# Kernel optimization log

Measured on AMD Instinct MI355X. Metric: run time of the kernel, lower is better.

The kernel has to match this reference:

```python
import jax, jax.numpy as jnp
import numpy as np

B, T, D, H, C = 64, 512, 128, 512, 256  # batch, seq_len, input_dim, rnn_dim, clf hidden


def _lstm_cell(x, h, c, Wih, Whh, b):
    # PyTorch gate order: i, f, g, o; b = bias_ih + bias_hh
    gates = x @ Wih.T + h @ Whh.T + b  # [B, 4H]
    i, f, g, o = jnp.split(gates, 4, axis=-1)
    c = jax.nn.sigmoid(f) * c + jax.nn.sigmoid(i) * jnp.tanh(g)
    h = jax.nn.sigmoid(o) * jnp.tanh(c)
    return h, c


def _run_lstm2(xs, state, p0, p1):
    # xs: [B, T, in]; state: (h0, c0, h1, c1) each [B, H]
    def step(carry, x_t):
        h0, c0, h1, c1 = carry
        h0, c0 = _lstm_cell(x_t, h0, c0, *p0)
        h1, c1 = _lstm_cell(h0, h1, c1, *p1)
        return (h0, c0, h1, c1), h1
    state, ys = jax.lax.scan(step, state, jnp.swapaxes(xs, 0, 1))
    return jnp.swapaxes(ys, 0, 1), state


def setup_inputs() -> dict:
    key = jax.random.key(0)
    ks = jax.random.split(key, 18)
    s = 0.04  # ~1/sqrt(H), matches torch LSTM init scale
    w = lambda k, shape: (jax.random.normal(k, shape, jnp.float32) * s)
    inp = {
        "x": jax.random.uniform(ks[0], (B, T, D), dtype=jnp.float32),
        "y": (jax.random.uniform(ks[1], (B, T, D), dtype=jnp.float32) > 0.9).astype(jnp.float32),
        "enc_Wih0": w(ks[2], (4 * H, D)), "enc_Whh0": w(ks[3], (4 * H, H)), "enc_b0": w(ks[4], (4 * H,)),
        "enc_Wih1": w(ks[5], (4 * H, H)), "enc_Whh1": w(ks[6], (4 * H, H)), "enc_b1": w(ks[7], (4 * H,)),
        "dec_Wih0": w(ks[8], (4 * H, D)), "dec_Whh0": w(ks[9], (4 * H, H)), "dec_b0": w(ks[10], (4 * H,)),
        "dec_Wih1": w(ks[11], (4 * H, H)), "dec_Whh1": w(ks[12], (4 * H, H)), "dec_b1": w(ks[13], (4 * H,)),
        "clf_W1": w(ks[14], (C, H)), "clf_b1": w(ks[15], (C,)),
        "clf_W2": w(ks[16], (D, C)), "clf_b2": w(ks[17], (D,)),
    }
    return inp


def reference(x, y, enc_Wih0, enc_Whh0, enc_b0, enc_Wih1, enc_Whh1, enc_b1,
              dec_Wih0, dec_Whh0, dec_b0, dec_Wih1, dec_Whh1, dec_b1,
              clf_W1, clf_b1, clf_W2, clf_b2):
    Bc = x.shape[0]
    z = jnp.zeros((Bc, H), x.dtype)
    # encoder: only final (h, c) of both layers is used
    _, state = _run_lstm2(x, (z, z, z, z),
                          (enc_Wih0, enc_Whh0, enc_b0), (enc_Wih1, enc_Whh1, enc_b1))
    # decoder under full teacher forcing: steps t=1..T-1 consume y[:, t-1]
    dec_out, _ = _run_lstm2(y[:, :-1], state,
                            (dec_Wih0, dec_Whh0, dec_b0), (dec_Wih1, dec_Whh1, dec_b1))
    hid = jax.nn.relu(dec_out @ clf_W1.T + clf_b1)          # [B, T-1, C]
    logits = hid @ clf_W2.T + clf_b2                        # [B, T-1, D]
    # outputs[:, 0] stays zero, as in the torch loop starting at t=1
    return jnp.concatenate([jnp.zeros_like(logits[:, :1]), logits], axis=1)
```

## Files before the change

### kernel.cpp

```cpp
#include <hip/hip_runtime.h>
#include <hip/hip_bf16.h>
#include <stdint.h>

#define SMEM_BYTES 150528

using short8  = __attribute__((ext_vector_type(8))) short;
using f32x4   = __attribute__((ext_vector_type(4))) float;
using u32x4   = __attribute__((ext_vector_type(4))) unsigned int;

#define OXBF 0u
#define OYBF 8388608u
#define OWE0 16777216u
#define OWD0 (OWE0 + 2621440u)
#define OWE1 (OWD0 + 2621440u)
#define OWD1 (OWE1 + 4194304u)
#define OWC1 (OWD1 + 4194304u)
#define OWC2 (OWC1 + 262144u)
#define OH0  (OWC2 + 65536u)
#define OH1  (OH0 + 524288u)
#define OHP  (OH1 + 524288u)
#define OFLG (OHP + 262144u)
#define OFC1 (OFLG + 4096u)
#define OFH  (OFLG + 8192u)
#define OFL  (OFLG + 9216u)
#define OH1B (OFLG + 16384u)

static __device__ __forceinline__ unsigned short f2bf(float f){
  union { float f; unsigned u; } v; v.f = f;
  unsigned r = v.u + 0x7FFFu + ((v.u >> 16) & 1u);
  return (unsigned short)(r >> 16);
}
static __device__ __forceinline__ float sigm(float x){ return 1.f/(1.f+__expf(-x)); }
static __device__ __forceinline__ float tanh_(float x){ return 1.f - 2.f/(__expf(2.f*x)+1.f); }

static __device__ __forceinline__ u32x4 ld_cg16(const void* p){
  u32x4 v;
  asm volatile("global_load_dwordx4 %0, %1, off sc0 sc1" : "=v"(v) : "v"(p) : "memory");
  return v;
}
static __device__ __forceinline__ unsigned ld_cg4(const void* p){
  unsigned v;
  asm volatile("global_load_dword %0, %1, off sc0 sc1\n\ts_waitcnt vmcnt(0)"
               : "=v"(v) : "v"(p) : "memory");
  return v;
}
static __device__ __forceinline__ void st_cg16(void* p, u32x4 v){
  asm volatile("global_store_dwordx4 %0, %1, off sc0 sc1" :: "v"(p), "v"(v) : "memory");
}
static __device__ __forceinline__ void st_cg4(void* p, unsigned v){
  asm volatile("global_store_dword %0, %1, off sc0 sc1" :: "v"(p), "v"(v) : "memory");
}
static __device__ __forceinline__ void drain_vm(){
  asm volatile("s_waitcnt vmcnt(0)" ::: "memory");
}
static __device__ __forceinline__ bool isS(u32x4 v){
  return (v[0]==0xFFFFFFFFu) | (v[1]==0xFFFFFFFFu) | (v[2]==0xFFFFFFFFu) | (v[3]==0xFFFFFFFFu);
}

__global__ void k_init(float* __restrict__ out, uint8_t* __restrict__ ws){
  int i = blockIdx.x*blockDim.x + threadIdx.x;
  int ns = gridDim.x*blockDim.x;
  uint32_t* r0 = (uint32_t*)(ws + OH0);
  uint32_t* r1 = (uint32_t*)(ws + OH1);
  const int slotw = 65536/4;
  for (int k=i; k<8*slotw; k+=ns){
    unsigned v = (k < 7*slotw) ? 0xFFFFFFFFu : 0u;
    r0[k] = v; r1[k] = v;
  }
  uint32_t* rb = (uint32_t*)(ws + OH1B);
  for (int k=i; k<8*slotw; k+=ns) rb[k] = 0xFFFFFFFFu;
  uint32_t* rp = (uint32_t*)(ws + OHP);
  for (int k=i; k<262144/4; k+=ns) rp[k] = 0xFFFFFFFFu;
  uint32_t* fl = (uint32_t*)(ws + OFLG);
  for (int k=i; k<16384/4; k+=ns) fl[k] = 0u;
  for (int k=i; k<64*128; k+=ns) out[(size_t)(k>>7)*(512*128) + (k&127)] = 0.f;
}

__global__ void k_cvt(const float* __restrict__ x, const float* __restrict__ y,
                      uint8_t* __restrict__ ws){
  unsigned short* xb = (unsigned short*)(ws + OXBF);
  unsigned short* yb = (unsigned short*)(ws + OYBF);
  const int n = 64*512*128;
  int i = blockIdx.x*blockDim.x + threadIdx.x, ns = gridDim.x*blockDim.x;
  for (int k=i; k<n; k+=ns){ xb[k] = f2bf(x[k]); yb[k] = f2bf(y[k]); }
}

__global__ void k_swzgate(const float* __restrict__ Wih, const float* __restrict__ Whh,
                          uint8_t* __restrict__ ws, size_t dstOff, int Kin, int KC, int NKK, int mode){
  unsigned short* dst = (unsigned short*)(ws + dstOff);
  const int total = 2048 * (KC*4);
  int i = blockIdx.x*blockDim.x + threadIdx.x, ns = gridDim.x*blockDim.x;
  for (int idx=i; idx<total; idx+=ns){
    int j = idx & 7;
    int lane = (idx >> 3) & 63;
    int t = idx >> 9;
    int g = t & 3; t >>= 2;
    int kk = t % NKK; t /= NKK;
    int w = t & 3; int ub = t >> 2;
    int off = ((lane>>4)<<3) + j;
    int k = mode ? (kk==0 ? w*32 + off : 128 + w*128 + (kk-1)*32 + off)
                 : (w*KC + kk*32 + off);
    int u = ub*16 + (lane&15);
    int row = g*512 + u;
    float v = (k < Kin) ? Wih[(size_t)row*Kin + k] : Whh[(size_t)row*512 + (k-Kin)];
    dst[idx] = f2bf(v);
  }
}

__global__ void k_swzclf(const float* __restrict__ W, uint8_t* __restrict__ ws,
                         size_t dstOff, int nwgs, int Kw, int Ktot){
  unsigned short* dst = (unsigned short*)(ws + dstOff);
  const int NKK = Kw/32;
  const int total = nwgs*4*NKK*64*8;
  int i = blockIdx.x*blockDim.x + threadIdx.x, ns = gridDim.x*blockDim.x;
  for (int idx=i; idx<total; idx+=ns){
    int j = idx & 7;
    int lane = (idx >> 3) & 63;
    int t = idx >> 9;
    int kk = t % NKK; t /= NKK;
    int w = t & 3; int wg = t >> 2;
    int k = w*Kw + kk*32 + ((lane>>4)<<3) + j;
    int col = wg*16 + (lane&15);
    dst[idx] = f2bf(W[(size_t)col*Ktot + k]);
  }
}

__launch_bounds__(256, 1)
__global__ void k_seq(uint8_t* __restrict__ ws,
                      const float* __restrict__ eb0, const float* __restrict__ eb1,
                      const float* __restrict__ db0, const float* __restrict__ db1,
                      const float* __restrict__ cb1, const float* __restrict__ cb2,
                      float* __restrict__ out){
  __shared__ uint8_t smem[SMEM_BYTES];
  const int wg = blockIdx.x, tid = threadIdx.x;
  const int w = tid>>6, l = tid&63, lr = l&15, lg = l>>4;

  const unsigned short* xb = (const unsigned short*)(ws+OXBF);
  const unsigned short* yb = (const unsigned short*)(ws+OYBF);
  unsigned short* h0r = (unsigned short*)(ws+OH0);
  unsigned short* h1r = (unsigned short*)(ws+OH1);
  unsigned short* h1b = (unsigned short*)(ws+OH1B);
  unsigned short* hpr = (unsigned short*)(ws+OHP);

  short8* BL = (short8*)smem;
  float*  P0 = (float*)(smem + 131072);
  float*  P1 = (float*)(smem + 139776);
  unsigned short* HS = (unsigned short*)(smem + 148480);

  const u32x4 S4 = (u32x4){0xFFFFFFFFu,0xFFFFFFFFu,0xFFFFFFFFu,0xFFFFFFFFu};

  auto loadB = [&](size_t srcOff, int bytes){
    const u32x4* s = (const u32x4*)(ws + srcOff);
    u32x4* d = (u32x4*)smem;
    for (int i = tid; i < bytes/16; i += 256) d[i] = s[i];
  };

  if (wg < 128){
    const bool isC0 = wg < 64;
    const int cwg = isC0 ? wg : wg-64;
    const int bt = cwg>>5, ub = cwg&31;
    const int u = tid&15, ug = ub*16 + u;
    const int bbytes = isC0 ? 81920 : 131072;

    float be[4], bd[4];
    {
      const float* e = isC0 ? eb0 : eb1;
      const float* d = isC0 ? db0 : db1;
      #pragma unroll
      for (int g=0; g<4; ++g){ be[g] = e[g*512+ug]; bd[g] = d[g*512+ug]; }
    }
    loadB((isC0 ? (size_t)OWE0 : (size_t)OWE1) + (size_t)ub*bbytes, bbytes);
    float cS0 = 0.f, cS1 = 0.f;
    __syncthreads();

    for (int t = 0; t < 1023; ++t){
      if (t == 512){
        __syncthreads();
        loadB((isC0 ? (size_t)OWD0 : (size_t)OWD1) + (size_t)ub*bbytes, bbytes);
        __syncthreads();
      }

      unsigned short* pub_base = isC0 ? h0r : ((t >= 512) ? h1b : h1r);
      unsigned short* clr_base = isC0 ? h0r : ((t+2 >= 512) ? h1b : h1r);

      if (w == 0){
        if (isC0){
          if (t >= 6 && l < 32){
            const void* p = ws + OFC1 + (size_t)(bt*32+l)*64;
            while ((int)ld_cg4(p) < t-5) __builtin_amdgcn_s_sleep(2);
          }
        } else {
          if (t >= 518 && l < 16){
            const void* p = ws + OFH + (size_t)l*64;
            while ((int)ld_cg4(p) < t-517) __builtin_amdgcn_s_sleep(2);
          }
        }
        const int cs = (t+2)&7, row = l>>1, half = l&1;
        st_cg16(clr_base + ((size_t)cs*64 + bt*32 + row)*512 + ub*16 + half*8, S4);
      }

      const int slotW = t&7, slotR = (t+7)&7;
      f32x4 acc[2][4];
      #pragma unroll
      for (int m=0;m<2;++m)
        #pragma unroll
        for (int g=0;g<4;++g) acc[m][g] = (f32x4){0.f,0.f,0.f,0.f};

      if (isC0){
        const unsigned short* xs = (t<512) ? xb : yb;
        const int tt = (t<512) ? t : t-512;
        short8 ax[2];
        #pragma unroll
        for (int m=0;m<2;++m){
          const int b = bt*32 + m*16 + lr;
          ax[m] = *(const short8*)(xs + ((size_t)b*512 + tt)*128 + w*32 + (lg<<3));
        }
        u32x4 ah[4][2];
        const unsigned short* base = h0r + (size_t)slotR*64*512;
        bool bad;
        do {
          #pragma unroll
          for (int kk=0; kk<4; ++kk)
            #pragma unroll
            for (int m=0;m<2;++m){
              const int b = bt*32 + m*16 + lr;
              ah[kk][m] = ld_cg16(base + (size_t)b*512 + w*128 + kk*32 + (lg<<3));
            }
          drain_vm();
          __builtin_amdgcn_sched_barrier(0);
          bad = false;
          #pragma unroll
          for (int kk=0; kk<4; ++kk)
            #pragma unroll
            for (int m=0;m<2;++m) bad |= isS(ah[kk][m]);
          if (bad) __builtin_amdgcn_s_sleep(1);
        } while (bad);
        __builtin_amdgcn_sched_barrier(0);
        #pragma unroll
        for (int g=0;g<4;++g){
          short8 bf = BL[((w*5+0)*4+g)*64 + l];
          acc[0][g] = __builtin_amdgcn_mfma_f32_16x16x32_bf16(ax[0], bf, acc[0][g],0,0,0);
          acc[1][g] = __builtin_amdgcn_mfma_f32_16x16x32_bf16(ax[1], bf, acc[1][g],0,0,0);
        }
        #pragma unroll
        for (int kk=1; kk<5; ++kk)
          #pragma unroll
          for (int g=0;g<4;++g){
            short8 bf = BL[((w*5+kk)*4+g)*64 + l];
            acc[0][g] = __builtin_amdgcn_mfma_f32_16x16x32_bf16(__builtin_bit_cast(short8, ah[kk-1][0]), bf, acc[0][g],0,0,0);
            acc[1][g] = __builtin_amdgcn_mfma_f32_16x16x32_bf16(__builtin_bit_cast(short8, ah[kk-1][1]), bf, acc[1][g],0,0,0);
          }
      } else {
        u32x4 a[8][2];
        const unsigned short* b0 = h0r + (size_t)slotW*64*512;
        const unsigned short* b1 = ((t-1 >= 512) ? h1b : h1r) + (size_t)slotR*64*512;
        bool bad;
        do {
          #pragma unroll
          for (int kk=0; kk<8; ++kk){
            const int k0 = w*256 + kk*32;
            #pragma unroll
            for (int m=0;m<2;++m){
              const int b = bt*32 + m*16 + lr;
              const void* ap = (k0 < 512)
                ? (const void*)(b0 + (size_t)b*512 + k0 + (lg<<3))
                : (const void*)(b1 + (size_t)b*512 + (k0-512) + (lg<<3));
              a[kk][m] = ld_cg16(ap);
            }
          }
          drain_vm();
          __builtin_amdgcn_sched_barrier(0);
          bad = false;
          #pragma unroll
          for (int kk=0; kk<8; ++kk)
            #pragma unroll
            for (int m=0;m<2;++m) bad |= isS(a[kk][m]);
          if (bad) __builtin_amdgcn_s_sleep(1);
        } while (bad);
        __builtin_amdgcn_sched_barrier(0);
        #pragma unroll
        for (int kk=0; kk<8; ++kk)
          #pragma unroll
          for (int g=0;g<4;++g){
            short8 bf = BL[((w*8+kk)*4+g)*64 + l];
            acc[0][g] = __builtin_amdgcn_mfma_f32_16x16x32_bf16(__builtin_bit_cast(short8, a[kk][0]), bf, acc[0][g],0,0,0);
            acc[1][g] = __builtin_amdgcn_mfma_f32_16x16x32_bf16(__builtin_bit_cast(short8, a[kk][1]), bf, acc[1][g],0,0,0);
          }
      }

      {
        float* P = (w&1) ? P1 : P0;
        if (w < 2){
          #pragma unroll
          for (int m=0;m<2;++m)
            #pragma unroll
            for (int g=0;g<4;++g)
              #pragma unroll
              for (int r=0;r<4;++r)
                P[(m*16 + (lg<<2) + r)*68 + g*16 + lr] = acc[m][g][r];
        }
        __syncthreads();
        if (w >= 2){
          #pragma unroll
          for (int m=0;m<2;++m)
            #pragma unroll
            for (int g=0;g<4;++g)
              #pragma unroll
              for (int r=0;r<4;++r)
                P[(m*16 + (lg<<2) + r)*68 + g*16 + lr] += acc[m][g][r];
        }
        __syncthreads();
      }

      const float* bias = (t<512) ? be : bd;
      #pragma unroll
      for (int s=0;s<2;++s){
        const int row = (tid>>4) + s*16;
        const int pi = row*68 + u;
        float gi = P0[pi]      + P1[pi]      + bias[0];
        float gf = P0[pi+16]   + P1[pi+16]   + bias[1];
        float gg = P0[pi+32]   + P1[pi+32]   + bias[2];
        float go = P0[pi+48]   + P1[pi+48]   + bias[3];
        float cprev = s ? cS1 : cS0;
        float c = sigm(gf)*cprev + sigm(gi)*tanh_(gg);
        if (s) cS1 = c; else cS0 = c;
        float h = sigm(go)*tanh_(c);
        HS[row*16 + u] = f2bf(h);
      }
      __syncthreads();
      if (tid < 64){
        u32x4 v = *(const u32x4*)(HS + tid*8);
        const int row = tid>>1, half = tid&1;
        st_cg16(pub_base + ((size_t)slotW*64 + bt*32 + row)*512 + ub*16 + half*8, v);
      }
      if (!isC0 && tid == 0)
        st_cg4(ws + OFC1 + (size_t)(bt*32+ub)*64, (unsigned)(t+1));
    }
  } else if (wg < 144){
    const int hwg = wg - 128;
    const int u = tid&15, col = hwg*16 + u;
    const float bc = cb1[col];
    loadB((size_t)OWC1 + (size_t)hwg*16384, 16384);
    __syncthreads();
    for (int t2 = 0; t2 < 511; ++t2){
      if (w == 0){
        if (t2 >= 6 && l < 8){
          const void* p = ws + OFL + (size_t)l*64;
          while ((int)ld_cg4(p) < t2-5) __builtin_amdgcn_s_sleep(2);
        }
        const int cs = (t2+2)&7;
        #pragma unroll
        for (int q=0;q<2;++q){
          const int i = l*2+q, row = i>>1, half = i&1;
          st_cg16(hpr + ((size_t)cs*64 + row)*256 + hwg*16 + half*8, S4);
        }
      }
      const int slot = t2&7;
      u32x4 a[4][4];
      const unsigned short* base = h1b + (size_t)slot*64*512;
      bool bad;
      do {
        #pragma unroll
        for (int kk=0; kk<4; ++kk)
          #pragma unroll
          for (int m=0;m<4;++m)
            a[kk][m] = ld_cg16(base + (size_t)(m*16+lr)*512 + w*128 + kk*32 + (lg<<3));
        drain_vm();
        __builtin_amdgcn_sched_barrier(0);
        bad = false;
        #pragma unroll
        for (int kk=0; kk<4; ++kk)
          #pragma unroll
          for (int m=0;m<4;++m) bad |= isS(a[kk][m]);
        if (bad) __builtin_amdgcn_s_sleep(1);
      } while (bad);
      __builtin_amdgcn_sched_barrier(0);
      f32x4 ha[4];
      #pragma unroll
      for (int m=0;m<4;++m) ha[m] = (f32x4){0.f,0.f,0.f,0.f};
      #pragma unroll
      for (int kk=0; kk<4; ++kk){
        short8 bf = BL[(w*4+kk)*64 + l];
        #pragma unroll
        for (int m=0;m<4;++m)
          ha[m] = __builtin_amdgcn_mfma_f32_16x16x32_bf16(__builtin_bit_cast(short8, a[kk][m]), bf, ha[m],0,0,0);
      }
      {
        float* P = (w&1) ? P1 : P0;
        if (w < 2){
          #pragma unroll
          for (int m=0;m<4;++m)
            #pragma unroll
            for (int r=0;r<4;++r)
              P[(m*16 + (lg<<2) + r)*20 + lr] = ha[m][r];
        }
        __syncthreads();
        if (w >= 2){
          #pragma unroll
          for (int m=0;m<4;++m)
            #pragma unroll
            for (int r=0;r<4;++r)
              P[(m*16 + (lg<<2) + r)*20 + lr] += ha[m][r];
        }
        __syncthreads();
      }
      #pragma unroll
      for (int s=0;s<4;++s){
        const int row = (tid>>4) + s*16;
        float v = P0[row*20+u] + P1[row*20+u] + bc;
        HS[row*16 + u] = f2bf(fmaxf(v, 0.f));
      }
      __syncthreads();
      if (tid < 128){
        u32x4 v = *(const u32x4*)(HS + tid*8);
        const int row = tid>>1, half = tid&1;
        st_cg16(hpr + ((size_t)slot*64 + row)*256 + hwg*16 + half*8, v);
      }
      if (tid == 0) st_cg4(ws + OFH + (size_t)hwg*64, (unsigned)(t2+1));
    }
  } else if (wg < 152){
    const int lwg = wg - 144;
    const int u = tid&15, col = lwg*16 + u;
    const float bc = cb2[col];
    loadB((size_t)OWC2 + (size_t)lwg*8192, 8192);
    __syncthreads();
    for (int t3 = 0; t3 < 511; ++t3){
      const int slot = t3&7;
      u32x4 a[2][4];
      const unsigned short* base = hpr + (size_t)slot*64*256;
      bool bad;
      do {
        #pragma unroll
        for (int kk=0; kk<2; ++kk)
          #pragma unroll
          for (int m=0;m<4;++m)
            a[kk][m] = ld_cg16(base + (size_t)(m*16+lr)*256 + w*64 + kk*32 + (lg<<3));
        drain_vm();
        __builtin_amdgcn_sched_barrier(0);
        bad = false;
        #pragma unroll
        for (int kk=0; kk<2; ++kk)
          #pragma unroll
          for (int m=0;m<4;++m) bad |= isS(a[kk][m]);
        if (bad) __builtin_amdgcn_s_sleep(1);
      } while (bad);
      __builtin_amdgcn_sched_barrier(0);
      f32x4 la[4];
      #pragma unroll
      for (int m=0;m<4;++m) la[m] = (f32x4){0.f,0.f,0.f,0.f};
      #pragma unroll
      for (int kk=0; kk<2; ++kk){
        short8 bf = BL[(w*2+kk)*64 + l];
        #pragma unroll
        for (int m=0;m<4;++m)
          la[m] = __builtin_amdgcn_mfma_f32_16x16x32_bf16(__builtin_bit_cast(short8, a[kk][m]), bf, la[m],0,0,0);
      }
      {
        float* P = (w&1) ? P1 : P0;
        if (w < 2){
          #pragma unroll
          for (int m=0;m<4;++m)
            #pragma unroll
            for (int r=0;r<4;++r)
              P[(m*16 + (lg<<2) + r)*20 + lr] = la[m][r];
        }
        __syncthreads();
        if (w >= 2){
          #pragma unroll
          for (int m=0;m<4;++m)
            #pragma unroll
            for (int r=0;r<4;++r)
              P[(m*16 + (lg<<2) + r)*20 + lr] += la[m][r];
        }
        __syncthreads();
      }
      #pragma unroll
      for (int s=0;s<4;++s){
        const int row = (tid>>4) + s*16;
        float v = P0[row*20+u] + P1[row*20+u] + bc;
        out[((size_t)row*512 + (t3+1))*128 + col] = v;
      }
      if (tid == 0) st_cg4(ws + OFL + (size_t)lwg*64, (unsigned)(t3+1));
    }
  }
}

extern "C" void kernel_launch(void* const* d_in, const int* in_sizes, int n_in,
                              void* d_out, int out_size, void* d_ws, size_t ws_size,
                              hipStream_t stream){
  const float* x   = (const float*)d_in[0];
  const float* y   = (const float*)d_in[1];
  const float* eW0 = (const float*)d_in[2];
  const float* eU0 = (const float*)d_in[3];
  const float* eb0 = (const float*)d_in[4];
  const float* eW1 = (const float*)d_in[5];
  const float* eU1 = (const float*)d_in[6];
  const float* eb1 = (const float*)d_in[7];
  const float* dW0 = (const float*)d_in[8];
  const float* dU0 = (const float*)d_in[9];
  const float* db0 = (const float*)d_in[10];
  const float* dW1 = (const float*)d_in[11];
  const float* dU1 = (const float*)d_in[12];
  const float* db1 = (const float*)d_in[13];
  const float* cW1 = (const float*)d_in[14];
  const float* cb1 = (const float*)d_in[15];
  const float* cW2 = (const float*)d_in[16];
  const float* cb2 = (const float*)d_in[17];
  float* out = (float*)d_out;
  uint8_t* ws = (uint8_t*)d_ws;
  (void)in_sizes; (void)n_in; (void)out_size; (void)ws_size;

  k_init<<<dim3(256), dim3(256), 0, stream>>>(out, ws);
  k_cvt<<<dim3(2048), dim3(256), 0, stream>>>(x, y, ws);
  k_swzgate<<<dim3(1280), dim3(256), 0, stream>>>(eW0, eU0, ws, (size_t)OWE0, 128, 160, 5, 1);
  k_swzgate<<<dim3(1280), dim3(256), 0, stream>>>(dW0, dU0, ws, (size_t)OWD0, 128, 160, 5, 1);
  k_swzgate<<<dim3(2048), dim3(256), 0, stream>>>(eW1, eU1, ws, (size_t)OWE1, 512, 256, 8, 0);
  k_swzgate<<<dim3(2048), dim3(256), 0, stream>>>(dW1, dU1, ws, (size_t)OWD1, 512, 256, 8, 0);
  k_swzclf<<<dim3(256), dim3(256), 0, stream>>>(cW1, ws, (size_t)OWC1, 16, 128, 512);
  k_swzclf<<<dim3(64),  dim3(256), 0, stream>>>(cW2, ws, (size_t)OWC2, 8, 64, 256);
  k_seq<<<dim3(152), dim3(256), 0, stream>>>(ws, eb0, eb1, db0, db1, cb1, cb2, out);
}
```

Before: 5.639 ms.

## Overlap consumer-progress flag polling with step compute and defer slot clearing

The per-step wait on downstream consumer flags and the sentinel clearing of ring-buffer slots are moved from before the matmul to after it. The flag load is issued asynchronously at the top of the step and only checked after the partial-sum reduction, and slots are cleared one step further ahead (t+3 instead of t+2). The intent is to take the flag-polling latency off the critical path of each recurrent step. In exchange the ring-buffer slack shrinks, which is a correctness risk if the index arithmetic is off.

```diff
diff --git a/kernel.cpp b/kernel.cpp
--- a/kernel.cpp
+++ b/kernel.cpp
@@ -42,6 +42,11 @@
   unsigned v;
   asm volatile("global_load_dword %0, %1, off sc0 sc1\n\ts_waitcnt vmcnt(0)"
                : "=v"(v) : "v"(p) : "memory");
+  return v;
+}
+static __device__ __forceinline__ unsigned ld_cg4_async(const void* p){
+  unsigned v;
+  asm volatile("global_load_dword %0, %1, off sc0 sc1" : "=v"(v) : "v"(p) : "memory");
   return v;
 }
 static __device__ __forceinline__ void st_cg16(void* p, u32x4 v){
@@ -180,26 +185,16 @@
         __syncthreads();
       }
 
+      const int slotW = t&7, slotR = (t+7)&7, slotC = (t+3)&7;
       unsigned short* pub_base = isC0 ? h0r : ((t >= 512) ? h1b : h1r);
-      unsigned short* clr_base = isC0 ? h0r : ((t+2 >= 512) ? h1b : h1r);
-
-      if (w == 0){
-        if (isC0){
-          if (t >= 6 && l < 32){
-            const void* p = ws + OFC1 + (size_t)(bt*32+l)*64;
-            while ((int)ld_cg4(p) < t-5) __builtin_amdgcn_s_sleep(2);
-          }
-        } else {
-          if (t >= 518 && l < 16){
-            const void* p = ws + OFH + (size_t)l*64;
-            while ((int)ld_cg4(p) < t-517) __builtin_amdgcn_s_sleep(2);
-          }
-        }
-        const int cs = (t+2)&7, row = l>>1, half = l&1;
-        st_cg16(clr_base + ((size_t)cs*64 + bt*32 + row)*512 + ub*16 + half*8, S4);
-      }
-
-      const int slotW = t&7, slotR = (t+7)&7;
+
+      const bool gateAct = isC0 ? (t >= 4) : (t >= 517);
+      const int  ng      = isC0 ? 32 : 16;
+      const void* fp = isC0 ? (const void*)(ws + OFC1 + (size_t)(bt*32 + (l&31))*64)
+                            : (const void*)(ws + OFH  + (size_t)(l&15)*64);
+      unsigned fv = 0u;
+      if (w == 0 && l < ng && gateAct) fv = ld_cg4_async(fp);
+
       f32x4 acc[2][4];
       #pragma unroll
       for (int m=0;m<2;++m)
@@ -310,6 +305,22 @@
                 P[(m*16 + (lg<<2) + r)*68 + g*16 + lr] += acc[m][g][r];
         }
         __syncthreads();
+      }
+
+      if (w == 0){
+        drain_vm();
+        __builtin_amdgcn_sched_barrier(0);
+        if (gateAct && l < ng){
+          const int n0 = isC0 ? (t-4) : (t-516);
+          const int need = (n0 < 1) ? 1 : n0;
+          int v = (int)fv;
+          while (v < need){ v = (int)ld_cg4(fp); __builtin_amdgcn_s_sleep(2); }
+        }
+        if (t >= 4 && t <= 1019){
+          unsigned short* cbase = isC0 ? h0r : ((t+3 >= 512) ? h1b : h1r);
+          const int row = l>>1, half = l&1;
+          st_cg16(cbase + ((size_t)slotC*64 + bt*32 + row)*512 + ub*16 + half*8, S4);
+        }
       }
 
       const float* bias = (t<512) ? be : bd;
@@ -343,19 +354,12 @@
     loadB((size_t)OWC1 + (size_t)hwg*16384, 16384);
     __syncthreads();
     for (int t2 = 0; t2 < 511; ++t2){
-      if (w == 0){
-        if (t2 >= 6 && l < 8){
-          const void* p = ws + OFL + (size_t)l*64;
-          while ((int)ld_cg4(p) < t2-5) __builtin_amdgcn_s_sleep(2);
-        }
-        const int cs = (t2+2)&7;
-        #pragma unroll
-        for (int q=0;q<2;++q){
-          const int i = l*2+q, row = i>>1, half = i&1;
-          st_cg16(hpr + ((size_t)cs*64 + row)*256 + hwg*16 + half*8, S4);
-        }
-      }
-      const int slot = t2&7;
+      const int slot = t2&7, slotC = (t2+3)&7;
+      const bool gateAct = (t2 >= 5);
+      const void* fp = (const void*)(ws + OFL + (size_t)(l&7)*64);
+      unsigned fv = 0u;
+      if (w == 0 && l < 8 && gateAct) fv = ld_cg4_async(fp);
+
       u32x4 a[4][4];
       const unsigned short* base = h1b + (size_t)slot*64*512;
       bool bad;
@@ -403,6 +407,21 @@
               P[(m*16 + (lg<<2) + r)*20 + lr] += ha[m][r];
         }
         __syncthreads();
+      }
+      if (w == 0){
+        drain_vm();
+        __builtin_amdgcn_sched_barrier(0);
+        if (gateAct && l < 8){
+          const int n0 = t2 - 4;
+          const int need = (n0 < 1) ? 1 : n0;
+          int v = (int)fv;
+          while (v < need){ v = (int)ld_cg4(fp); __builtin_amdgcn_s_sleep(2); }
+        }
+        if (t2 >= 5 && t2 <= 507){
+          #pragma unroll
+          for (int q=0;q<2;++q)
+            st_cg16(hpr + ((size_t)slotC*64 + l)*256 + hwg*16 + q*8, S4);
+        }
       }
       #pragma unroll
       for (int s=0;s<4;++s){
```

Result: slower. 5.779 ms (+2.5%).
